# Kernel tuning notes

Measured on AMD Instinct MI355X. Metric: run time of the kernel, lower is better.

The kernel has to match this reference:

```python
import jax, jax.numpy as jnp
import numpy as np

ROPE_BASE = 10000.0
CHUNK = 2048
NEG_INF = -1e30


def _rope(q, k, start_index):
    # q, k: (B, T, H, Dh) with Dh even; half-split RoPE as in RotaryEmbedding
    B, T, H, Dh = q.shape
    half = Dh // 2
    inv_freq = jnp.exp(jnp.arange(half, dtype=jnp.float32) * (-(np.log(ROPE_BASE) / half)))
    pos = jnp.arange(T, dtype=jnp.float32) + jnp.float32(start_index)
    ang = pos[:, None] * inv_freq[None, :]              # (T, half)
    cos = jnp.cos(ang)[None, :, None, :].astype(q.dtype)  # (1,T,1,half)
    sin = jnp.sin(ang)[None, :, None, :].astype(q.dtype)

    def rot(x):
        x1, x2 = x[..., :half], x[..., half:]
        return jnp.concatenate([x1 * cos - x2 * sin, x2 * cos + x1 * sin], axis=-1)

    return rot(q), rot(k)


def reference(q, k, v, start_index):
    # Chunked causal self-attention, softmax(QK^T) V with scale = 1.0 (Megalodon Eq. 9).
    B, T, H, Dh = q.shape
    Dv = v.shape[-1]
    q, k = _rope(q, k, start_index)

    nc = T // CHUNK  # T assumed multiple of chunk_size (prefill path, no cache)
    qc = q.reshape(B, nc, CHUNK, H, Dh)
    kc = k.reshape(B, nc, CHUNK, H, Dh)
    vc = v.reshape(B, nc, CHUNK, H, Dv)

    # per-chunk causal mask (C, C): 0 where j <= i else -inf
    i = jnp.arange(CHUNK)
    causal = (i[None, :] <= i[:, None])

    scores = jnp.einsum('bnqhd,bnkhd->bnhqk', qc, kc)  # scale = 1.0
    scores = jnp.where(causal[None, None, None, :, :], scores, NEG_INF)
    probs = jax.nn.softmax(scores, axis=-1)
    out = jnp.einsum('bnhqk,bnkhd->bnqhd', probs, vc)
    return out.reshape(B, T, H, Dv)


def setup_inputs() -> dict:
    key = jax.random.key(0)
    kq, kk, kv = jax.random.split(key, 3)
    B, T, H, Dh, Dv = 2, 4096, 16, 128, 128
    return {
        'q': jax.random.normal(kq, (B, T, H, Dh), dtype=jnp.float32),
        'k': jax.random.normal(kk, (B, T, H, Dh), dtype=jnp.float32),
        'v': jax.random.normal(kv, (B, T, H, Dv), dtype=jnp.float32),
        'start_index': 0,
    }
```

## Files before the change

kernel.cpp:

```cpp
#include <hip/hip_runtime.h>


#define T_TOT  4096
#define HH     16
#define DH     128
#define CHUNKL 2048
#define QT     128
#define KTILE  64
#define KTB    128
#define NEGV   1e30f
#define L2E    1.44269504088896f
#define THRL2  11.5415603f

typedef _Float16 f16;
typedef __attribute__((ext_vector_type(8)))  _Float16 f16x8;
typedef __attribute__((ext_vector_type(4)))  _Float16 f16x4;
typedef __attribute__((ext_vector_type(2)))  _Float16 f16x2;
typedef __attribute__((ext_vector_type(4)))  float    f32x4;
typedef __attribute__((ext_vector_type(16))) float    f32x16;
typedef __attribute__((ext_vector_type(4)))  int      i32x4;

#define AS_G(p) ((const __attribute__((address_space(1))) void*)(p))
#define AS_L(p) ((__attribute__((address_space(3))) void*)(p))

__device__ __forceinline__ f32x16 mfma32(f16x8 a, f16x8 b, f32x16 c) {
    return __builtin_amdgcn_mfma_f32_32x32x16_f16(a, b, c, 0, 0, 0);
}
__device__ __forceinline__ f32x4 mfma16(f16x8 a, f16x8 b, f32x4 c) {
    return __builtin_amdgcn_mfma_f32_16x16x32_f16(a, b, c, 0, 0, 0);
}
__device__ __forceinline__ int pk2(float a, float b) {
    f16x2 t; t[0] = (f16)a; t[1] = (f16)b;
    return __builtin_bit_cast(int, t);
}

__global__ void rope_table_kernel(float* __restrict__ tab, const int* __restrict__ startp) {
    int gid = blockIdx.x * blockDim.x + threadIdx.x;
    int t = gid >> 6, d = gid & 63;
    float pos  = (float)(t + *startp);
    float invf = expf((float)d * (-9.210340371976184f / 64.0f));
    float s, c;
    sincosf(pos * invf, &s, &c);
    tab[gid] = c;
    tab[T_TOT * 64 + gid] = s;
}

__global__ void prep_kv_kernel(const float* __restrict__ K, const float* __restrict__ V,
                               const float* __restrict__ tab,
                               f16* __restrict__ Kws, f16* __restrict__ VTws) {
    const int half = (2 * T_TOT * HH * DH) / 8;
    int gid = blockIdx.x * blockDim.x + threadIdx.x;
    if (gid < half) {
        const int tile = gid >> 11, idx = gid & 2047;
        const int key = idx >> 4, c8 = idx & 15;
        const int dsw0 = c8 << 3;
        const int sw   = (key & 7) << 3;
        const int d0   = dsw0 ^ sw;
        const int kt = tile & 15, h = (tile >> 4) & 15, n = (tile >> 8) & 1, b = tile >> 9;
        const int t  = n * CHUNKL + kt * KTB + key;
        const float* kp = K + ((size_t)(b * T_TOT + t) * HH + h) * DH;
        const int dl = d0 & 63;
        f32x4 xm0 = *(const f32x4*)(kp + d0);
        f32x4 xm1 = *(const f32x4*)(kp + d0 + 4);
        f32x4 xo0 = *(const f32x4*)(kp + (d0 ^ 64));
        f32x4 xo1 = *(const f32x4*)(kp + (d0 ^ 64) + 4);
        f32x4 cc0 = *(const f32x4*)(tab + t * 64 + dl);
        f32x4 cc1 = *(const f32x4*)(tab + t * 64 + dl + 4);
        f32x4 ss0 = *(const f32x4*)(tab + T_TOT * 64 + t * 64 + dl);
        f32x4 ss1 = *(const f32x4*)(tab + T_TOT * 64 + t * 64 + dl + 4);
        const float sgn = (d0 < 64) ? -1.f : 1.f;
        f16x8 out;
#pragma unroll
        for (int j = 0; j < 4; ++j) {
            out[j]     = (f16)(xm0[j] * cc0[j] + sgn * xo0[j] * ss0[j]);
            out[4 + j] = (f16)(xm1[j] * cc1[j] + sgn * xo1[j] * ss1[j]);
        }
        *(f16x8*)&Kws[(size_t)tile * 16384 + key * DH + dsw0] = out;
    } else {
        const int oc = gid - half;
        const int tile = oc >> 11, idx = oc & 2047;
        const int d = idx >> 4, c8 = idx & 15;
        const int ksw0 = c8 << 3;
        const int sw   = (d & 7) << 3;
        const int key0 = ksw0 ^ sw;
        const int kt = tile & 15, h = (tile >> 4) & 15, n = (tile >> 8) & 1, b = tile >> 9;
        const int t0 = n * CHUNKL + kt * KTB + key0;
        const float* vp = V + ((size_t)(b * T_TOT + t0) * HH + h) * DH + d;
        f16x8 out;
#pragma unroll
        for (int j = 0; j < 8; ++j)
            out[j] = (f16)vp[(size_t)j * (HH * DH)];
        *(f16x8*)&VTws[(size_t)tile * 16384 + d * KTB + ksw0] = out;
    }
}

__global__ __launch_bounds__(512, 2)
void attn_fast_kernel(const float* __restrict__ Q, const f16* __restrict__ Kws,
                      const f16* __restrict__ VTws, const float* __restrict__ tab,
                      float* __restrict__ O)
{
    __shared__ f16 Kl[2][KTB * DH];
    __shared__ f16 VTl[2][KTB * DH];

    const int bid = blockIdx.x;
    const int sb  = (bid & 7) * 64 + (bid >> 3);
    const int pr  = sb & 7;
    const int bnh = sb >> 3;
    const int hd = bnh & 15, n = (bnh >> 4) & 1, b = bnh >> 5;
    const int qtA = pr, qtB = 15 - pr;

    const int tid = threadIdx.x;
    const int w   = tid >> 6;
    const int wq  = w & 3;
    const int l   = tid & 63;
    const int hl  = l >> 5;
    const int c31 = l & 31;

    const int qt_w = (w < 4) ? qtA : qtB;
    const int q0   = qt_w * QT;
    const size_t bh = (size_t)b * T_TOT * (HH * DH) + (size_t)hd * DH;
    const size_t tile0 = (size_t)bnh * (16 * 16384);

    const int qr = q0 + wq * 32 + c31;
    const int tg = n * CHUNKL + qr;
    const float* qp = Q + bh + (size_t)tg * (HH * DH);

    f16x8 qf[8];
#pragma unroll
    for (int ks = 0; ks < 8; ++ks) {
        const int dbase = ks * 16 + 8 * hl;
        const int dl    = dbase & 63;
        f32x4 xa0 = *(const f32x4*)(qp + dbase);
        f32x4 xa1 = *(const f32x4*)(qp + dbase + 4);
        f32x4 xb0 = *(const f32x4*)(qp + (dbase ^ 64));
        f32x4 xb1 = *(const f32x4*)(qp + (dbase ^ 64) + 4);
        float cc[8], ss[8];
        *(f32x4*)&cc[0] = *(const f32x4*)(tab + tg * 64 + dl);
        *(f32x4*)&cc[4] = *(const f32x4*)(tab + tg * 64 + dl + 4);
        *(f32x4*)&ss[0] = *(const f32x4*)(tab + T_TOT * 64 + tg * 64 + dl);
        *(f32x4*)&ss[4] = *(const f32x4*)(tab + T_TOT * 64 + tg * 64 + dl + 4);
        const float sgn = (dbase < 64) ? -1.f : 1.f;
        float xa[8] = {xa0[0],xa0[1],xa0[2],xa0[3],xa1[0],xa1[1],xa1[2],xa1[3]};
        float xb[8] = {xb0[0],xb0[1],xb0[2],xb0[3],xb1[0],xb1[1],xb1[2],xb1[3]};
        f16x8 f;
#pragma unroll
        for (int j = 0; j < 8; ++j)
            f[j] = (f16)((xa[j] * cc[j] + sgn * xb[j] * ss[j]) * L2E);
        qf[ks] = f;
    }

    f32x16 o[4];
    float mrun = -NEGV, lrun = 0.f;
#pragma unroll
    for (int dt = 0; dt < 4; ++dt)
#pragma unroll
        for (int r = 0; r < 16; ++r) o[dt][r] = 0.f;

    const int nkt = qtB + 1;

#define STAGE_TILE(t, bufi)                                                              \
    do {                                                                                 \
        const f16* ks_ = Kws  + tile0 + (size_t)(t) * 16384;                             \
        const f16* vs_ = VTws + tile0 + (size_t)(t) * 16384;                             \
        _Pragma("unroll")                                                                \
        for (int i = 0; i < 4; ++i) {                                                    \
            const int off = (i * 8 + w) * 512;                                           \
            __builtin_amdgcn_global_load_lds(AS_G(ks_ + off + l * 8),                    \
                                             AS_L(&Kl[bufi][off]),  16, 0, 0);           \
            __builtin_amdgcn_global_load_lds(AS_G(vs_ + off + l * 8),                    \
                                             AS_L(&VTl[bufi][off]), 16, 0, 0);           \
        }                                                                                \
    } while (0)

    STAGE_TILE(0, 0);
    STAGE_TILE(1, 1);

    for (int kt = 0; kt < nkt; ++kt) {
        if (kt + 1 < nkt) {
            asm volatile("s_waitcnt vmcnt(8)" ::: "memory");
        } else {
            asm volatile("s_waitcnt vmcnt(0)" ::: "memory");
        }
        __builtin_amdgcn_s_barrier();
        __builtin_amdgcn_sched_barrier(0);

        const int cur = kt & 1;
        const bool active = (kt * KTB) < (q0 + wq * 32 + 32);
        if (active) {
            const f16* Klc  = Kl[cur];
            const f16* VTlc = VTl[cur];

            f32x16 s[4];
#pragma unroll
            for (int ts = 0; ts < 4; ++ts)
#pragma unroll
                for (int r = 0; r < 16; ++r) s[ts][r] = 0.f;

            __builtin_amdgcn_s_setprio(1);
#pragma unroll
            for (int ks = 0; ks < 8; ++ks) {
#pragma unroll
                for (int ts = 0; ts < 4; ++ts) {
                    const int key = ts * 32 + c31;
                    const int swk = (key & 7) << 3;
                    f16x8 kf = *(const f16x8*)&Klc[key * DH + ((ks * 16 + 8 * hl) ^ swk)];
                    s[ts] = mfma32(kf, qf[ks], s[ts]);
                }
            }
            __builtin_amdgcn_s_setprio(0);

            if (kt == qt_w) {
#pragma unroll
                for (int ts = 0; ts < 4; ++ts)
#pragma unroll
                    for (int r = 0; r < 16; ++r) {
                        const int key = kt * KTB + ts * 32 + (r & 3) + 8 * (r >> 2) + 4 * hl;
                        if (key > qr) s[ts][r] = -NEGV;
                    }
            }

            float mx = s[0][0];
#pragma unroll
            for (int ts = 0; ts < 4; ++ts)
#pragma unroll
                for (int r = 0; r < 16; ++r) mx = fmaxf(mx, s[ts][r]);
            mx = fmaxf(mx, __shfl_xor(mx, 32));

            if (__any(mx > mrun + THRL2)) {
                const float mn = fmaxf(mrun, mx);
                const float al = exp2f(mrun - mn);
                mrun = mn;
                lrun *= al;
#pragma unroll
                for (int dt = 0; dt < 4; ++dt)
#pragma unroll
                    for (int r = 0; r < 16; ++r) o[dt][r] *= al;
            }

            float ps = 0.f;
#pragma unroll
            for (int ts = 0; ts < 4; ++ts)
#pragma unroll
                for (int r = 0; r < 16; ++r) {
                    const float p = exp2f(s[ts][r] - mrun);
                    s[ts][r] = p;
                    ps += p;
                }
            lrun += ps;

            __builtin_amdgcn_s_setprio(1);
#pragma unroll
            for (int ts = 0; ts < 4; ++ts) {
                f16x8 pbg[2];
#pragma unroll
                for (int gs = 0; gs < 2; ++gs) {
                    const int G = 8 * gs;
                    const int A  = pk2(s[ts][G + 0], s[ts][G + 1]);
                    const int Bw = pk2(s[ts][G + 2], s[ts][G + 3]);
                    const int C  = pk2(s[ts][G + 4], s[ts][G + 5]);
                    const int Dw = pk2(s[ts][G + 6], s[ts][G + 7]);
                    const int Y1 = hl ? A : C;
                    const int Y2 = hl ? Bw : Dw;
                    const int r1 = __shfl_xor(Y1, 32);
                    const int r2 = __shfl_xor(Y2, 32);
                    i32x4 bi;
                    bi[0] = hl ? r1 : A;
                    bi[1] = hl ? r2 : Bw;
                    bi[2] = hl ? C  : r1;
                    bi[3] = hl ? Dw : r2;
                    pbg[gs] = __builtin_bit_cast(f16x8, bi);
                }
#pragma unroll
                for (int dt = 0; dt < 4; ++dt) {
                    const int d   = dt * 32 + c31;
                    const int swv = (d & 7) << 3;
                    f16x8 vf0 = *(const f16x8*)&VTlc[d * KTB + (((2 * ts) * 16 + 8 * hl) ^ swv)];
                    o[dt] = mfma32(vf0, pbg[0], o[dt]);
                    f16x8 vf1 = *(const f16x8*)&VTlc[d * KTB + (((2 * ts + 1) * 16 + 8 * hl) ^ swv)];
                    o[dt] = mfma32(vf1, pbg[1], o[dt]);
                }
            }
            __builtin_amdgcn_s_setprio(0);
        }

        __builtin_amdgcn_s_barrier();
        if (kt + 2 < nkt) STAGE_TILE(kt + 2, cur);
    }
#undef STAGE_TILE

    const float lt  = lrun + __shfl_xor(lrun, 32);
    const float inv = 1.0f / lt;
    float* op = O + bh + (size_t)tg * (HH * DH);
#pragma unroll
    for (int dt = 0; dt < 4; ++dt) {
#pragma unroll
        for (int dd = 0; dd < 4; ++dd) {
            f32x4 val;
#pragma unroll
            for (int c = 0; c < 4; ++c) val[c] = o[dt][4 * dd + c] * inv;
            *(f32x4*)&op[dt * 32 + dd * 8 + 4 * hl] = val;
        }
    }
}

__global__ __launch_bounds__(256, 2)
void attn_kernel(const float* __restrict__ Q, const float* __restrict__ K,
                 const float* __restrict__ V, const int* __restrict__ startp,
                 float* __restrict__ O)
{
    __shared__ f16 Kl[KTILE * DH];
    __shared__ f16 VTl[DH * KTILE];
    __shared__ f16 Pl[4][32 * 72];

    const int bid = blockIdx.x;
    const int qt  = 15 - (bid & 15);
    const int bnh = bid >> 4;
    const int h = bnh & 15, n = (bnh >> 4) & 1, b = bnh >> 5;

    const int tid  = threadIdx.x;
    const int w    = tid >> 6;
    const int lane = tid & 63;
    const int g    = lane >> 4, m = lane & 15;

    const int q0 = qt * QT;
    const size_t bh = (size_t)b * T_TOT * (HH * DH) + (size_t)h * DH;
    const int start = *startp;

    f16x8  qf[2][4];
    float  mrun[2][4], lrun[2][4];
    f32x4  o[2][8];
    const f32x4 ZERO4 = {0.f, 0.f, 0.f, 0.f};

#pragma unroll
    for (int rs = 0; rs < 2; ++rs) {
#pragma unroll
        for (int r = 0; r < 4; ++r) { mrun[rs][r] = -NEGV; lrun[rs][r] = 0.f; }
#pragma unroll
        for (int dt = 0; dt < 8; ++dt) o[rs][dt] = ZERO4;

        const int tg = n * CHUNKL + q0 + w * 32 + rs * 16 + m;
        const float* qp = Q + bh + (size_t)tg * (HH * DH);
#pragma unroll
        for (int kc = 0; kc < 4; ++kc) {
            const int dbase = kc * 32 + g * 8;
            const int dlo   = dbase & 63;
            f32x4 xa0 = *(const f32x4*)(qp + dbase);
            f32x4 xa1 = *(const f32x4*)(qp + dbase + 4);
            f32x4 xb0 = *(const f32x4*)(qp + (dbase ^ 64));
            f32x4 xb1 = *(const f32x4*)(qp + (dbase ^ 64) + 4);
            float cc[8], ss[8];
#pragma unroll
            for (int j = 0; j < 8; ++j) {
                float invf = expf((float)(dlo + j) * (-9.210340371976184f / 64.0f));
                sincosf((float)(tg + start) * invf, &ss[j], &cc[j]);
            }
            const float sgn = (dbase < 64) ? -1.f : 1.f;
            float xa[8] = {xa0[0],xa0[1],xa0[2],xa0[3],xa1[0],xa1[1],xa1[2],xa1[3]};
            float xb[8] = {xb0[0],xb0[1],xb0[2],xb0[3],xb1[0],xb1[1],xb1[2],xb1[3]};
            f16x8 f;
#pragma unroll
            for (int j = 0; j < 8; ++j) f[j] = (f16)(xa[j] * cc[j] + sgn * xb[j] * ss[j]);
            qf[rs][kc] = f;
        }
    }

    const int nkt = 2 * qt + 2;
    for (int kt = 0; kt < nkt; ++kt) {
        __syncthreads();
#pragma unroll
        for (int it = 0; it < 4; ++it) {
            const int tau = tid + 256 * it;
            const int row = tau >> 4;
            const int d0  = (tau & 15) << 2;
            const int tg  = n * CHUNKL + kt * KTILE + row;
            const float* kp = K + bh + (size_t)tg * (HH * DH);
            f32x4 xa = *(const f32x4*)(kp + d0);
            f32x4 xb = *(const f32x4*)(kp + d0 + 64);
            f32x4 cc, ss;
#pragma unroll
            for (int j = 0; j < 4; ++j) {
                float invf = expf((float)(d0 + j) * (-9.210340371976184f / 64.0f));
                float sv, cv;
                sincosf((float)(tg + start) * invf, &sv, &cv);
                cc[j] = cv; ss[j] = sv;
            }
            f16x4 oA, oB;
#pragma unroll
            for (int j = 0; j < 4; ++j) {
                oA[j] = (f16)(xa[j] * cc[j] - xb[j] * ss[j]);
                oB[j] = (f16)(xb[j] * cc[j] + xa[j] * ss[j]);
            }
            const int sw = (row & 7) << 3;
            *(f16x4*)&Kl[row * DH + (d0 ^ sw)]        = oA;
            *(f16x4*)&Kl[row * DH + ((d0 + 64) ^ sw)] = oB;
        }
#pragma unroll
        for (int it = 0; it < 8; ++it) {
            const int tau = tid + 256 * it;
            const int key = tau & 63;
            const int d0  = (tau >> 6) << 2;
            const int tg  = n * CHUNKL + kt * KTILE + key;
            f32x4 x = *(const f32x4*)(V + bh + (size_t)tg * (HH * DH) + d0);
#pragma unroll
            for (int j = 0; j < 4; ++j) {
                const int d = d0 + j;
                VTl[d * KTILE + (key ^ ((d & 7) << 3))] = (f16)x[j];
            }
        }
        __syncthreads();

        const bool active = (kt * KTILE) < (q0 + w * 32 + 32);
        if (active) {
            f32x4 sa[2][4];
#pragma unroll
            for (int rs = 0; rs < 2; ++rs)
#pragma unroll
                for (int nt = 0; nt < 4; ++nt) sa[rs][nt] = ZERO4;
#pragma unroll
            for (int nt = 0; nt < 4; ++nt) {
                const int key = nt * 16 + m;
                const int swk = (key & 7) << 3;
#pragma unroll
                for (int kc = 0; kc < 4; ++kc) {
                    f16x8 bf = *(const f16x8*)&Kl[key * DH + ((kc * 32 + g * 8) ^ swk)];
                    sa[0][nt] = mfma16(qf[0][kc], bf, sa[0][nt]);
                    sa[1][nt] = mfma16(qf[1][kc], bf, sa[1][nt]);
                }
            }
            const bool domask = (kt >= 2 * qt);
#pragma unroll
            for (int rs = 0; rs < 2; ++rs) {
                if (domask) {
#pragma unroll
                    for (int nt = 0; nt < 4; ++nt) {
                        const int key = kt * KTILE + nt * 16 + m;
#pragma unroll
                        for (int r = 0; r < 4; ++r) {
                            const int qr = q0 + w * 32 + rs * 16 + 4 * g + r;
                            if (key > qr) sa[rs][nt][r] = -NEGV;
                        }
                    }
                }
                float mx[4];
#pragma unroll
                for (int r = 0; r < 4; ++r)
                    mx[r] = fmaxf(fmaxf(sa[rs][0][r], sa[rs][1][r]),
                                  fmaxf(sa[rs][2][r], sa[rs][3][r]));
#pragma unroll
                for (int off = 1; off < 16; off <<= 1)
#pragma unroll
                    for (int r = 0; r < 4; ++r)
                        mx[r] = fmaxf(mx[r], __shfl_xor(mx[r], off));
                float al[4], ps[4];
#pragma unroll
                for (int r = 0; r < 4; ++r) {
                    const float mn = fmaxf(mrun[rs][r], mx[r]);
                    al[r] = exp2f((mrun[rs][r] - mn) * L2E);
                    mrun[rs][r] = mn;
                    ps[r] = 0.f;
                }
#pragma unroll
                for (int nt = 0; nt < 4; ++nt)
#pragma unroll
                    for (int r = 0; r < 4; ++r) {
                        const float p = exp2f((sa[rs][nt][r] - mrun[rs][r]) * L2E);
                        sa[rs][nt][r] = p;
                        ps[r] += p;
                    }
#pragma unroll
                for (int off = 1; off < 16; off <<= 1)
#pragma unroll
                    for (int r = 0; r < 4; ++r)
                        ps[r] += __shfl_xor(ps[r], off);
#pragma unroll
                for (int r = 0; r < 4; ++r)
                    lrun[rs][r] = lrun[rs][r] * al[r] + ps[r];
#pragma unroll
                for (int dt = 0; dt < 8; ++dt)
#pragma unroll
                    for (int r = 0; r < 4; ++r)
                        o[rs][dt][r] *= al[r];
#pragma unroll
                for (int nt = 0; nt < 4; ++nt)
#pragma unroll
                    for (int r = 0; r < 4; ++r)
                        Pl[w][(rs * 16 + 4 * g + r) * 72 + nt * 16 + m] = (f16)sa[rs][nt][r];
            }
            f16x8 pa[2][2];
#pragma unroll
            for (int rs = 0; rs < 2; ++rs)
#pragma unroll
                for (int kc = 0; kc < 2; ++kc)
                    pa[rs][kc] = *(const f16x8*)&Pl[w][(rs * 16 + m) * 72 + kc * 32 + g * 8];
#pragma unroll
            for (int dt = 0; dt < 8; ++dt) {
                const int d   = dt * 16 + m;
                const int swv = (d & 7) << 3;
#pragma unroll
                for (int kc = 0; kc < 2; ++kc) {
                    f16x8 vf = *(const f16x8*)&VTl[d * KTILE + ((kc * 32 + g * 8) ^ swv)];
                    o[0][dt] = mfma16(pa[0][kc], vf, o[0][dt]);
                    o[1][dt] = mfma16(pa[1][kc], vf, o[1][dt]);
                }
            }
        }
    }

#pragma unroll
    for (int rs = 0; rs < 2; ++rs) {
#pragma unroll
        for (int r = 0; r < 4; ++r) {
            const float inv = 1.0f / lrun[rs][r];
            const int tg = n * CHUNKL + q0 + w * 32 + rs * 16 + 4 * g + r;
            float* op = O + bh + (size_t)tg * (HH * DH);
#pragma unroll
            for (int dt = 0; dt < 8; ++dt)
                op[dt * 16 + m] = o[rs][dt][r] * inv;
        }
    }
}

extern "C" void kernel_launch(void* const* d_in, const int* in_sizes, int n_in,
                              void* d_out, int out_size, void* d_ws, size_t ws_size,
                              hipStream_t stream) {
    const float* q = (const float*)d_in[0];
    const float* k = (const float*)d_in[1];
    const float* v = (const float*)d_in[2];
    const int* start = (const int*)d_in[3];
    float* out = (float*)d_out;

    const size_t tab_elems = (size_t)2 * T_TOT * 64;
    const size_t kv_elems  = (size_t)2 * T_TOT * HH * DH;
    const size_t need = tab_elems * sizeof(float) + 2 * kv_elems * sizeof(f16);

    if (ws_size >= need) {
        float* tab = (float*)d_ws;
        f16* Kws  = (f16*)((char*)d_ws + tab_elems * sizeof(float));
        f16* VTws = Kws + kv_elems;
        rope_table_kernel<<<(T_TOT * 64) / 256, 256, 0, stream>>>(tab, start);
        prep_kv_kernel<<<(int)(2 * (kv_elems / 8) / 256), 256, 0, stream>>>(k, v, tab, Kws, VTws);
        attn_fast_kernel<<<512, 512, 0, stream>>>(q, Kws, VTws, tab, out);
    } else {
        attn_kernel<<<64 * 16, 256, 0, stream>>>(q, k, v, start, out);
    }
}
```

Baseline: 223.4 us.

## Switch fast attention to 16x16 MFMA tiles with 64-key K/V tiles

Rewrites the fast attention kernel to use 16x16x32 MFMA instead of 32x32x16, with each wave owning 16 query rows and K/V staged in 64-key tiles. Each block now handles a single 128-row Q tile rather than a balanced pair, and the grid grows to 1024 blocks. P is routed through a per-wave swizzled LDS buffer instead of being rearranged with cross-lane shuffles. The prep kernel is changed to emit the matching 64-key tile layout with new swizzles. The smaller LDS footprint and launch bounds allow more resident blocks per CU, at the cost of losing the paired load balancing and adding LDS traffic for P.

```diff
diff --git a/kernel.cpp b/kernel.cpp
--- a/kernel.cpp
+++ b/kernel.cpp
@@ -7,7 +7,6 @@
 #define CHUNKL 2048
 #define QT     128
 #define KTILE  64
-#define KTB    128
 #define NEGV   1e30f
 #define L2E    1.44269504088896f
 #define THRL2  11.5415603f
@@ -15,23 +14,13 @@
 typedef _Float16 f16;
 typedef __attribute__((ext_vector_type(8)))  _Float16 f16x8;
 typedef __attribute__((ext_vector_type(4)))  _Float16 f16x4;
-typedef __attribute__((ext_vector_type(2)))  _Float16 f16x2;
 typedef __attribute__((ext_vector_type(4)))  float    f32x4;
-typedef __attribute__((ext_vector_type(16))) float    f32x16;
-typedef __attribute__((ext_vector_type(4)))  int      i32x4;
 
 #define AS_G(p) ((const __attribute__((address_space(1))) void*)(p))
 #define AS_L(p) ((__attribute__((address_space(3))) void*)(p))
 
-__device__ __forceinline__ f32x16 mfma32(f16x8 a, f16x8 b, f32x16 c) {
-    return __builtin_amdgcn_mfma_f32_32x32x16_f16(a, b, c, 0, 0, 0);
-}
 __device__ __forceinline__ f32x4 mfma16(f16x8 a, f16x8 b, f32x4 c) {
     return __builtin_amdgcn_mfma_f32_16x16x32_f16(a, b, c, 0, 0, 0);
-}
-__device__ __forceinline__ int pk2(float a, float b) {
-    f16x2 t; t[0] = (f16)a; t[1] = (f16)b;
-    return __builtin_bit_cast(int, t);
 }
 
 __global__ void rope_table_kernel(float* __restrict__ tab, const int* __restrict__ startp) {
@@ -51,13 +40,12 @@
     const int half = (2 * T_TOT * HH * DH) / 8;
     int gid = blockIdx.x * blockDim.x + threadIdx.x;
     if (gid < half) {
-        const int tile = gid >> 11, idx = gid & 2047;
+        const int tile = gid >> 10, idx = gid & 1023;
         const int key = idx >> 4, c8 = idx & 15;
         const int dsw0 = c8 << 3;
-        const int sw   = (key & 7) << 3;
-        const int d0   = dsw0 ^ sw;
-        const int kt = tile & 15, h = (tile >> 4) & 15, n = (tile >> 8) & 1, b = tile >> 9;
-        const int t  = n * CHUNKL + kt * KTB + key;
+        const int d0   = dsw0 ^ ((key & 15) << 3);
+        const int kt = tile & 31, h = (tile >> 5) & 15, n = (tile >> 9) & 1, b = tile >> 10;
+        const int t  = n * CHUNKL + kt * KTILE + key;
         const float* kp = K + ((size_t)(b * T_TOT + t) * HH + h) * DH;
         const int dl = d0 & 63;
         f32x4 xm0 = *(const f32x4*)(kp + d0);
@@ -75,60 +63,57 @@
             out[j]     = (f16)(xm0[j] * cc0[j] + sgn * xo0[j] * ss0[j]);
             out[4 + j] = (f16)(xm1[j] * cc1[j] + sgn * xo1[j] * ss1[j]);
         }
-        *(f16x8*)&Kws[(size_t)tile * 16384 + key * DH + dsw0] = out;
+        *(f16x8*)&Kws[(size_t)tile * 8192 + key * DH + dsw0] = out;
     } else {
         const int oc = gid - half;
-        const int tile = oc >> 11, idx = oc & 2047;
-        const int d = idx >> 4, c8 = idx & 15;
+        const int tile = oc >> 10, idx = oc & 1023;
+        const int d = idx >> 3, c8 = idx & 7;
         const int ksw0 = c8 << 3;
-        const int sw   = (d & 7) << 3;
-        const int key0 = ksw0 ^ sw;
-        const int kt = tile & 15, h = (tile >> 4) & 15, n = (tile >> 8) & 1, b = tile >> 9;
-        const int t0 = n * CHUNKL + kt * KTB + key0;
+        const int key0 = ksw0 ^ ((d & 7) << 3);
+        const int kt = tile & 31, h = (tile >> 5) & 15, n = (tile >> 9) & 1, b = tile >> 10;
+        const int t0 = n * CHUNKL + kt * KTILE + key0;
         const float* vp = V + ((size_t)(b * T_TOT + t0) * HH + h) * DH + d;
         f16x8 out;
 #pragma unroll
         for (int j = 0; j < 8; ++j)
             out[j] = (f16)vp[(size_t)j * (HH * DH)];
-        *(f16x8*)&VTws[(size_t)tile * 16384 + d * KTB + ksw0] = out;
+        *(f16x8*)&VTws[(size_t)tile * 8192 + d * KTILE + ksw0] = out;
     }
 }
 
-__global__ __launch_bounds__(512, 2)
+__global__ __launch_bounds__(512, 4)
 void attn_fast_kernel(const float* __restrict__ Q, const f16* __restrict__ Kws,
                       const f16* __restrict__ VTws, const float* __restrict__ tab,
                       float* __restrict__ O)
 {
-    __shared__ f16 Kl[2][KTB * DH];
-    __shared__ f16 VTl[2][KTB * DH];
+    __shared__ f16 Kl[2][KTILE * DH];
+    __shared__ f16 VTl[2][KTILE * DH];
+    __shared__ f16 Pl[8][16 * 64];
 
     const int bid = blockIdx.x;
-    const int sb  = (bid & 7) * 64 + (bid >> 3);
-    const int pr  = sb & 7;
-    const int bnh = sb >> 3;
+    const int sb  = (bid & 7) * 128 + (bid >> 3);
+    const int qt  = 15 - (sb & 15);
+    const int bnh = sb >> 4;
     const int hd = bnh & 15, n = (bnh >> 4) & 1, b = bnh >> 5;
-    const int qtA = pr, qtB = 15 - pr;
 
     const int tid = threadIdx.x;
     const int w   = tid >> 6;
-    const int wq  = w & 3;
     const int l   = tid & 63;
-    const int hl  = l >> 5;
-    const int c31 = l & 31;
-
-    const int qt_w = (w < 4) ? qtA : qtB;
-    const int q0   = qt_w * QT;
+    const int g   = l >> 4;
+    const int m   = l & 15;
+
+    const int q0 = qt * QT;
     const size_t bh = (size_t)b * T_TOT * (HH * DH) + (size_t)hd * DH;
-    const size_t tile0 = (size_t)bnh * (16 * 16384);
-
-    const int qr = q0 + wq * 32 + c31;
+    const size_t tile0 = (size_t)bnh * (32 * 8192);
+
+    const int qr = q0 + w * 16 + m;
     const int tg = n * CHUNKL + qr;
     const float* qp = Q + bh + (size_t)tg * (HH * DH);
 
-    f16x8 qf[8];
-#pragma unroll
-    for (int ks = 0; ks < 8; ++ks) {
-        const int dbase = ks * 16 + 8 * hl;
+    f16x8 qf[4];
+#pragma unroll
+    for (int kc = 0; kc < 4; ++kc) {
+        const int dbase = kc * 32 + g * 8;
         const int dl    = dbase & 63;
         f32x4 xa0 = *(const f32x4*)(qp + dbase);
         f32x4 xa1 = *(const f32x4*)(qp + dbase + 4);
@@ -146,30 +131,29 @@
 #pragma unroll
         for (int j = 0; j < 8; ++j)
             f[j] = (f16)((xa[j] * cc[j] + sgn * xb[j] * ss[j]) * L2E);
-        qf[ks] = f;
-    }
-
-    f32x16 o[4];
+        qf[kc] = f;
+    }
+
+    f32x4 o[8];
     float mrun = -NEGV, lrun = 0.f;
-#pragma unroll
-    for (int dt = 0; dt < 4; ++dt)
-#pragma unroll
-        for (int r = 0; r < 16; ++r) o[dt][r] = 0.f;
-
-    const int nkt = qtB + 1;
+    const f32x4 ZERO4 = {0.f, 0.f, 0.f, 0.f};
+#pragma unroll
+    for (int dt = 0; dt < 8; ++dt) o[dt] = ZERO4;
+
+    const int nkt = 2 * qt + 2;
 
 #define STAGE_TILE(t, bufi)                                                              \
     do {                                                                                 \
-        const f16* ks_ = Kws  + tile0 + (size_t)(t) * 16384;                             \
-        const f16* vs_ = VTws + tile0 + (size_t)(t) * 16384;                             \
-        _Pragma("unroll")                                                                \
-        for (int i = 0; i < 4; ++i) {                                                    \
-            const int off = (i * 8 + w) * 512;                                           \
-            __builtin_amdgcn_global_load_lds(AS_G(ks_ + off + l * 8),                    \
-                                             AS_L(&Kl[bufi][off]),  16, 0, 0);           \
-            __builtin_amdgcn_global_load_lds(AS_G(vs_ + off + l * 8),                    \
-                                             AS_L(&VTl[bufi][off]), 16, 0, 0);           \
-        }                                                                                \
+        const f16* ks_ = Kws  + tile0 + (size_t)(t) * 8192;                              \
+        const f16* vs_ = VTws + tile0 + (size_t)(t) * 8192;                              \
+        __builtin_amdgcn_global_load_lds(AS_G(ks_ + tid * 8),                            \
+                                         AS_L(&Kl[bufi][tid * 8]), 16, 0, 0);            \
+        __builtin_amdgcn_global_load_lds(AS_G(ks_ + 4096 + tid * 8),                     \
+                                         AS_L(&Kl[bufi][4096 + tid * 8]), 16, 0, 0);     \
+        __builtin_amdgcn_global_load_lds(AS_G(vs_ + tid * 8),                            \
+                                         AS_L(&VTl[bufi][tid * 8]), 16, 0, 0);           \
+        __builtin_amdgcn_global_load_lds(AS_G(vs_ + 4096 + tid * 8),                     \
+                                         AS_L(&VTl[bufi][4096 + tid * 8]), 16, 0, 0);    \
     } while (0)
 
     STAGE_TILE(0, 0);
@@ -177,7 +161,7 @@
 
     for (int kt = 0; kt < nkt; ++kt) {
         if (kt + 1 < nkt) {
-            asm volatile("s_waitcnt vmcnt(8)" ::: "memory");
+            asm volatile("s_waitcnt vmcnt(4)" ::: "memory");
         } else {
             asm volatile("s_waitcnt vmcnt(0)" ::: "memory");
         }
@@ -185,45 +169,43 @@
         __builtin_amdgcn_sched_barrier(0);
 
         const int cur = kt & 1;
-        const bool active = (kt * KTB) < (q0 + wq * 32 + 32);
+        const bool active = (kt * KTILE) < (q0 + w * 16 + 16);
         if (active) {
             const f16* Klc  = Kl[cur];
             const f16* VTlc = VTl[cur];
 
-            f32x16 s[4];
-#pragma unroll
-            for (int ts = 0; ts < 4; ++ts)
-#pragma unroll
-                for (int r = 0; r < 16; ++r) s[ts][r] = 0.f;
+            f32x4 s[4];
+#pragma unroll
+            for (int ts = 0; ts < 4; ++ts) s[ts] = ZERO4;
 
             __builtin_amdgcn_s_setprio(1);
 #pragma unroll
-            for (int ks = 0; ks < 8; ++ks) {
+            for (int kc = 0; kc < 4; ++kc) {
 #pragma unroll
                 for (int ts = 0; ts < 4; ++ts) {
-                    const int key = ts * 32 + c31;
-                    const int swk = (key & 7) << 3;
-                    f16x8 kf = *(const f16x8*)&Klc[key * DH + ((ks * 16 + 8 * hl) ^ swk)];
-                    s[ts] = mfma32(kf, qf[ks], s[ts]);
+                    const int key = ts * 16 + m;
+                    f16x8 kf = *(const f16x8*)&Klc[key * DH + ((kc * 32 + 8 * g) ^ (m * 8))];
+                    s[ts] = mfma16(kf, qf[kc], s[ts]);
                 }
             }
             __builtin_amdgcn_s_setprio(0);
 
-            if (kt == qt_w) {
+            if ((kt + 1) * KTILE > q0 + w * 16) {
 #pragma unroll
                 for (int ts = 0; ts < 4; ++ts)
 #pragma unroll
-                    for (int r = 0; r < 16; ++r) {
-                        const int key = kt * KTB + ts * 32 + (r & 3) + 8 * (r >> 2) + 4 * hl;
+                    for (int r = 0; r < 4; ++r) {
+                        const int key = kt * KTILE + ts * 16 + 4 * g + r;
                         if (key > qr) s[ts][r] = -NEGV;
                     }
             }
 
-            float mx = s[0][0];
-#pragma unroll
-            for (int ts = 0; ts < 4; ++ts)
-#pragma unroll
-                for (int r = 0; r < 16; ++r) mx = fmaxf(mx, s[ts][r]);
+            float mx0 = fmaxf(fmaxf(s[0][0], s[0][1]), fmaxf(s[0][2], s[0][3]));
+            float mx1 = fmaxf(fmaxf(s[1][0], s[1][1]), fmaxf(s[1][2], s[1][3]));
+            float mx2 = fmaxf(fmaxf(s[2][0], s[2][1]), fmaxf(s[2][2], s[2][3]));
+            float mx3 = fmaxf(fmaxf(s[3][0], s[3][1]), fmaxf(s[3][2], s[3][3]));
+            float mx  = fmaxf(fmaxf(mx0, mx1), fmaxf(mx2, mx3));
+            mx = fmaxf(mx, __shfl_xor(mx, 16));
             mx = fmaxf(mx, __shfl_xor(mx, 32));
 
             if (__any(mx > mrun + THRL2)) {
@@ -232,52 +214,43 @@
                 mrun = mn;
                 lrun *= al;
 #pragma unroll
-                for (int dt = 0; dt < 4; ++dt)
-#pragma unroll
-                    for (int r = 0; r < 16; ++r) o[dt][r] *= al;
-            }
-
-            float ps = 0.f;
+                for (int dt = 0; dt < 8; ++dt)
+#pragma unroll
+                    for (int r = 0; r < 4; ++r) o[dt][r] *= al;
+            }
+
 #pragma unroll
             for (int ts = 0; ts < 4; ++ts)
 #pragma unroll
-                for (int r = 0; r < 16; ++r) {
-                    const float p = exp2f(s[ts][r] - mrun);
-                    s[ts][r] = p;
-                    ps += p;
-                }
-            lrun += ps;
+                for (int r = 0; r < 4; ++r) s[ts][r] = exp2f(s[ts][r] - mrun);
+            {
+                float p0 = (s[0][0] + s[0][1]) + (s[0][2] + s[0][3]);
+                float p1 = (s[1][0] + s[1][1]) + (s[1][2] + s[1][3]);
+                float p2 = (s[2][0] + s[2][1]) + (s[2][2] + s[2][3]);
+                float p3 = (s[3][0] + s[3][1]) + (s[3][2] + s[3][3]);
+                lrun += (p0 + p1) + (p2 + p3);
+            }
+
+#pragma unroll
+            for (int ts = 0; ts < 4; ++ts) {
+                f16x4 pk;
+                pk[0] = (f16)s[ts][0];
+                pk[1] = (f16)s[ts][1];
+                pk[2] = (f16)s[ts][2];
+                pk[3] = (f16)s[ts][3];
+                const int blk = (2 * ts + (g >> 1)) ^ (m & 7);
+                *(f16x4*)&Pl[w][m * 64 + blk * 8 + (g & 1) * 4] = pk;
+            }
 
             __builtin_amdgcn_s_setprio(1);
 #pragma unroll
-            for (int ts = 0; ts < 4; ++ts) {
-                f16x8 pbg[2];
-#pragma unroll
-                for (int gs = 0; gs < 2; ++gs) {
-                    const int G = 8 * gs;
-                    const int A  = pk2(s[ts][G + 0], s[ts][G + 1]);
-                    const int Bw = pk2(s[ts][G + 2], s[ts][G + 3]);
-                    const int C  = pk2(s[ts][G + 4], s[ts][G + 5]);
-                    const int Dw = pk2(s[ts][G + 6], s[ts][G + 7]);
-                    const int Y1 = hl ? A : C;
-                    const int Y2 = hl ? Bw : Dw;
-                    const int r1 = __shfl_xor(Y1, 32);
-                    const int r2 = __shfl_xor(Y2, 32);
-                    i32x4 bi;
-                    bi[0] = hl ? r1 : A;
-                    bi[1] = hl ? r2 : Bw;
-                    bi[2] = hl ? C  : r1;
-                    bi[3] = hl ? Dw : r2;
-                    pbg[gs] = __builtin_bit_cast(f16x8, bi);
-                }
-#pragma unroll
-                for (int dt = 0; dt < 4; ++dt) {
-                    const int d   = dt * 32 + c31;
-                    const int swv = (d & 7) << 3;
-                    f16x8 vf0 = *(const f16x8*)&VTlc[d * KTB + (((2 * ts) * 16 + 8 * hl) ^ swv)];
-                    o[dt] = mfma32(vf0, pbg[0], o[dt]);
-                    f16x8 vf1 = *(const f16x8*)&VTlc[d * KTB + (((2 * ts + 1) * 16 + 8 * hl) ^ swv)];
-                    o[dt] = mfma32(vf1, pbg[1], o[dt]);
+            for (int kc = 0; kc < 2; ++kc) {
+                f16x8 pb = *(const f16x8*)&Pl[w][m * 64 + ((kc * 4 + g) ^ (m & 7)) * 8];
+#pragma unroll
+                for (int dt = 0; dt < 8; ++dt) {
+                    const int d = dt * 16 + m;
+                    f16x8 vf = *(const f16x8*)&VTlc[d * KTILE + ((kc * 32 + 8 * g) ^ ((m & 7) * 8))];
+                    o[dt] = mfma16(vf, pb, o[dt]);
                 }
             }
             __builtin_amdgcn_s_setprio(0);
@@ -288,18 +261,17 @@
     }
 #undef STAGE_TILE
 
-    const float lt  = lrun + __shfl_xor(lrun, 32);
+    float lt = lrun;
+    lt += __shfl_xor(lt, 16);
+    lt += __shfl_xor(lt, 32);
     const float inv = 1.0f / lt;
     float* op = O + bh + (size_t)tg * (HH * DH);
 #pragma unroll
-    for (int dt = 0; dt < 4; ++dt) {
-#pragma unroll
-        for (int dd = 0; dd < 4; ++dd) {
-            f32x4 val;
-#pragma unroll
-            for (int c = 0; c < 4; ++c) val[c] = o[dt][4 * dd + c] * inv;
-            *(f32x4*)&op[dt * 32 + dd * 8 + 4 * hl] = val;
-        }
+    for (int dt = 0; dt < 8; ++dt) {
+        f32x4 val;
+#pragma unroll
+        for (int r = 0; r < 4; ++r) val[r] = o[dt][r] * inv;
+        *(f32x4*)&op[dt * 16 + 4 * g] = val;
     }
 }
 
@@ -539,7 +511,7 @@
         f16* VTws = Kws + kv_elems;
         rope_table_kernel<<<(T_TOT * 64) / 256, 256, 0, stream>>>(tab, start);
         prep_kv_kernel<<<(int)(2 * (kv_elems / 8) / 256), 256, 0, stream>>>(k, v, tab, Kws, VTws);
-        attn_fast_kernel<<<512, 512, 0, stream>>>(q, Kws, VTws, tab, out);
+        attn_fast_kernel<<<1024, 512, 0, stream>>>(q, Kws, VTws, tab, out);
     } else {
         attn_kernel<<<64 * 16, 256, 0, stream>>>(q, k, v, start, out);
     }
```

After: 210.3 us. -5.9%, faster.
